# Optimization experiments

Measured on AMD Instinct MI355X. Metric: run time of the kernel, lower is better.

Reference implementation:

```python
import jax, jax.numpy as jnp
import numpy as np

# Math of ExampleModelSISO (in float; GMACv2 with unit scalars reduces to add,
# GMACv2([x],[y],[]) to elementwise multiply, CastToPrecision to identity):
#   states s_i (i=0..num_states-1) all init to zeros and all update identically:
#       s_i[t+1] = x[t] + s_i[t]
#   per-step output is x[t] * s_last[t], where s_last[t] = sum_{k<t} x[k]
#   i.e. out[t] = x[t] * exclusive_cumsum(x)[t]  (over the time axis).
# All num_states states are identical, so the scan collapses to one exclusive
# cumulative sum along time — fully vectorized, memory-bound.

def setup_inputs() -> dict:
    key = jax.random.key(0)
    B, T, D = 8, 4096, 1024
    x = jax.random.normal(key, (B, T, D), dtype=jnp.float32)
    return {"x": x}

def reference(x) -> jnp.ndarray:
    # exclusive cumulative sum over time axis (state before current input is added)
    prev_state = jnp.cumsum(x, axis=1) - x  # [B, T, D]
    return x * prev_state
```

## Files before the change

### kernel.cpp

```cpp
#include <hip/hip_runtime.h>


typedef float vf4 __attribute__((ext_vector_type(4)));

constexpr int B = 8;
constexpr int T = 4096;
constexpr int D = 1024;
constexpr int C = 128;
constexpr int L = T / C;
constexpr int THREADS = 256;
constexpr int BD = B * D;

__global__ __launch_bounds__(THREADS)
void partial_sums(const float* __restrict__ x, float* __restrict__ part) {
    const int bc = blockIdx.x;
    const int b = bc / C;
    const int c = bc % C;
    const int d4 = threadIdx.x * 4;

    const float* px = x + ((size_t)(b * T + c * L)) * D + d4;
    vf4 acc = (vf4)(0.f);
#pragma unroll 8
    for (int t = 0; t < L; ++t) {
        vf4 v = *(const vf4*)(px + (size_t)t * D);
        acc += v;
    }
    *(vf4*)(part + (size_t)c * BD + b * D + d4) = acc;
}

__global__ __launch_bounds__(THREADS)
void scan_partials(float* __restrict__ part) {
    const int j = blockIdx.x * blockDim.x + threadIdx.x;
    float run = 0.f;
    constexpr int TILE = 16;
#pragma unroll
    for (int c0 = 0; c0 < C; c0 += TILE) {
        float v[TILE];
#pragma unroll
        for (int k = 0; k < TILE; ++k)
            v[k] = part[(size_t)(c0 + k) * BD + j];
#pragma unroll
        for (int k = 0; k < TILE; ++k) {
            part[(size_t)(c0 + k) * BD + j] = run;
            run += v[k];
        }
    }
}

__global__ __launch_bounds__(THREADS)
void scan_mul(const float* __restrict__ x, const float* __restrict__ part,
              float* __restrict__ out) {
    const int bc = blockIdx.x;
    const int b = bc / C;
    const int c = bc % C;
    const int d4 = threadIdx.x * 4;

    const size_t base = ((size_t)(b * T + c * L)) * D + d4;
    vf4 s = *(const vf4*)(part + (size_t)c * BD + b * D + d4);
#pragma unroll 4
    for (int t = 0; t < L; ++t) {
        vf4 v = *(const vf4*)(x + base + (size_t)t * D);
        vf4 o = v * s;
        s += v;
        __builtin_nontemporal_store(o, (vf4*)(out + base + (size_t)t * D));
    }
}

extern "C" void kernel_launch(void* const* d_in, const int* in_sizes, int n_in,
                              void* d_out, int out_size, void* d_ws, size_t ws_size,
                              hipStream_t stream) {
    const float* x = (const float*)d_in[0];
    float* out = (float*)d_out;
    float* part = (float*)d_ws;

    partial_sums<<<B * C, THREADS, 0, stream>>>(x, part);
    scan_partials<<<BD / THREADS, THREADS, 0, stream>>>(part);
    scan_mul<<<B * C, THREADS, 0, stream>>>(x, part, out);
}
```

Baseline: 254.4 us.

## Replace three-pass scan with single-pass decoupled look-back scan

Merges the partial-sum, partial-scan and multiply kernels into one kernel. Chunks are assigned through an atomic ticket counter, and each chunk publishes a flagged aggregate or inclusive prefix in 64-bit slots that later chunks poll with a look-back. The second read of x for a chunk happens right after its first read, so it is likely served from cache, which aims to remove most of the extra full pass over x and two kernel launches. In exchange it adds an init kernel to clear the flags, spin-waiting on predecessors with a bounded retry count, and larger workspace traffic from the 64-bit slots.

```diff
diff --git a/kernel.cpp b/kernel.cpp
--- a/kernel.cpp
+++ b/kernel.cpp
@@ -9,71 +9,134 @@
 constexpr int C = 128;
 constexpr int L = T / C;
 constexpr int THREADS = 256;
-constexpr int BD = B * D;
+constexpr int NCHUNK = B * C;
+
+constexpr unsigned FLAG_INVALID = 0u;
+constexpr unsigned FLAG_AGG     = 1u;
+constexpr unsigned FLAG_PREFIX  = 2u;
+
 
 __global__ __launch_bounds__(THREADS)
-void partial_sums(const float* __restrict__ x, float* __restrict__ part) {
-    const int bc = blockIdx.x;
-    const int b = bc / C;
-    const int c = bc % C;
-    const int d4 = threadIdx.x * 4;
-
-    const float* px = x + ((size_t)(b * T + c * L)) * D + d4;
-    vf4 acc = (vf4)(0.f);
-#pragma unroll 8
-    for (int t = 0; t < L; ++t) {
-        vf4 v = *(const vf4*)(px + (size_t)t * D);
-        acc += v;
-    }
-    *(vf4*)(part + (size_t)c * BD + b * D + d4) = acc;
+void init_state(unsigned long long* __restrict__ slots,
+                unsigned* __restrict__ counter) {
+    const size_t i = (size_t)blockIdx.x * THREADS + threadIdx.x;
+#pragma unroll
+    for (int k = 0; k < 4; ++k)
+        slots[i * 4 + k] = 0ULL;
+    if (i == 0) *counter = 0u;
 }
 
 __global__ __launch_bounds__(THREADS)
-void scan_partials(float* __restrict__ part) {
-    const int j = blockIdx.x * blockDim.x + threadIdx.x;
-    float run = 0.f;
-    constexpr int TILE = 16;
+void scan_lookback(const float* __restrict__ x, float* __restrict__ out,
+                   unsigned long long* __restrict__ slots,
+                   unsigned* __restrict__ counter) {
+    __shared__ unsigned s_ticket;
+    if (threadIdx.x == 0) s_ticket = atomicAdd(counter, 1u);
+    __syncthreads();
+    const unsigned v = s_ticket;
+    const int b = (int)(v & (B - 1));
+    const int c = (int)(v >> 3);
+    const int d4 = threadIdx.x * 4;
+
+    const size_t xbase = ((size_t)(b * T + c * L)) * D + d4;
+
+    vf4 agg = (vf4)(0.f);
+#pragma unroll 8
+    for (int t = 0; t < L; ++t)
+        agg += *(const vf4*)(x + xbase + (size_t)t * D);
+
+    unsigned long long* myslot = slots + ((size_t)c * B + b) * D + d4;
+    {
+        const unsigned long long f =
+            (unsigned long long)(c == 0 ? FLAG_PREFIX : FLAG_AGG) << 32;
 #pragma unroll
-    for (int c0 = 0; c0 < C; c0 += TILE) {
-        float v[TILE];
-#pragma unroll
-        for (int k = 0; k < TILE; ++k)
-            v[k] = part[(size_t)(c0 + k) * BD + j];
-#pragma unroll
-        for (int k = 0; k < TILE; ++k) {
-            part[(size_t)(c0 + k) * BD + j] = run;
-            run += v[k];
+        for (int j = 0; j < 4; ++j) {
+            unsigned long long pk =
+                f | (unsigned long long)__float_as_uint(agg[j]);
+            __hip_atomic_store(&myslot[j], pk, __ATOMIC_RELAXED,
+                               __HIP_MEMORY_SCOPE_AGENT);
         }
     }
-}
 
-__global__ __launch_bounds__(THREADS)
-void scan_mul(const float* __restrict__ x, const float* __restrict__ part,
-              float* __restrict__ out) {
-    const int bc = blockIdx.x;
-    const int b = bc / C;
-    const int c = bc % C;
-    const int d4 = threadIdx.x * 4;
+    float pref[4] = {0.f, 0.f, 0.f, 0.f};
+    if (c > 0) {
+        int P = c - 1;
+        unsigned pend = 0xFu;
+        unsigned rounds = 0u;
+        while (pend) {
+            if (++rounds > (1u << 22)) break;
+            unsigned long long sv[4][4];
+#pragma unroll
+            for (int k = 0; k < 4; ++k) {
+                int p = P - k;
+                p = p < 0 ? 0 : p;
+                const unsigned long long* ps =
+                    slots + ((size_t)p * B + b) * D + d4;
+#pragma unroll
+                for (int j = 0; j < 4; ++j)
+                    sv[k][j] = __hip_atomic_load(&ps[j], __ATOMIC_RELAXED,
+                                                 __HIP_MEMORY_SCOPE_AGENT);
+            }
+            int consumed = 0;
+            bool halt = false;
+#pragma unroll
+            for (int k = 0; k < 4; ++k) {
+                const bool active = !halt && (P - k >= 0) && (pend != 0u);
+                if (active) {
+                    unsigned rdy = 1u;
+#pragma unroll
+                    for (int j = 0; j < 4; ++j)
+                        if ((pend >> j) & 1u)
+                            if ((unsigned)(sv[k][j] >> 32) == FLAG_INVALID)
+                                rdy = 0u;
+                    if (!rdy) {
+                        halt = true;
+                    } else {
+#pragma unroll
+                        for (int j = 0; j < 4; ++j)
+                            if ((pend >> j) & 1u) {
+                                pref[j] += __uint_as_float(
+                                    (unsigned)(sv[k][j] & 0xffffffffULL));
+                                if ((unsigned)(sv[k][j] >> 32) == FLAG_PREFIX)
+                                    pend &= ~(1u << j);
+                            }
+                        ++consumed;
+                    }
+                }
+            }
+            P -= consumed;
+            if (consumed == 0 && pend) __builtin_amdgcn_s_sleep(1);
+        }
+        const unsigned long long f = (unsigned long long)FLAG_PREFIX << 32;
+#pragma unroll
+        for (int j = 0; j < 4; ++j) {
+            unsigned long long pk =
+                f | (unsigned long long)__float_as_uint(pref[j] + agg[j]);
+            __hip_atomic_store(&myslot[j], pk, __ATOMIC_RELAXED,
+                               __HIP_MEMORY_SCOPE_AGENT);
+        }
+    }
 
-    const size_t base = ((size_t)(b * T + c * L)) * D + d4;
-    vf4 s = *(const vf4*)(part + (size_t)c * BD + b * D + d4);
+    vf4 s;
+    s[0] = pref[0]; s[1] = pref[1]; s[2] = pref[2]; s[3] = pref[3];
 #pragma unroll 4
     for (int t = 0; t < L; ++t) {
-        vf4 v = *(const vf4*)(x + base + (size_t)t * D);
-        vf4 o = v * s;
-        s += v;
-        __builtin_nontemporal_store(o, (vf4*)(out + base + (size_t)t * D));
+        vf4 vv = *(const vf4*)(x + xbase + (size_t)t * D);
+        vf4 o = vv * s;
+        s += vv;
+        __builtin_nontemporal_store(o, (vf4*)(out + xbase + (size_t)t * D));
     }
 }
 
 extern "C" void kernel_launch(void* const* d_in, const int* in_sizes, int n_in,
-                              void* d_out, int out_size, void* d_ws, size_t ws_size,
-                              hipStream_t stream) {
+                              void* d_out, int out_size, void* d_ws,
+                              size_t ws_size, hipStream_t stream) {
     const float* x = (const float*)d_in[0];
     float* out = (float*)d_out;
-    float* part = (float*)d_ws;
+    unsigned long long* slots = (unsigned long long*)d_ws;
+    unsigned* counter =
+        (unsigned*)((char*)d_ws + (size_t)NCHUNK * D * sizeof(unsigned long long));
 
-    partial_sums<<<B * C, THREADS, 0, stream>>>(x, part);
-    scan_partials<<<BD / THREADS, THREADS, 0, stream>>>(part);
-    scan_mul<<<B * C, THREADS, 0, stream>>>(x, part, out);
+    init_state<<<1024, THREADS, 0, stream>>>(slots, counter);
+    scan_lookback<<<NCHUNK, THREADS, 0, stream>>>(x, out, slots, counter);
 }
```

Measured after the change: 612.3 us. 141% more time.

## Fuse three scan kernels into one cooperative kernel with grid syncs

Applied to the files above, without the earlier changes.

Merges the partial-sum, partial-scan and scan-multiply kernels into a single cooperative launch separated by two grid-wide barriers. This removes two kernel launch gaps. Each block's chunk of x may also still be in L2/MALL when it is reread in the final pass. In exchange it adds grid.sync overhead, and only 32 of the 1024 blocks do the middle scan while the rest wait. The cooperative launch also requires all blocks to be co-resident.

```diff
diff --git a/kernel.cpp b/kernel.cpp
--- a/kernel.cpp
+++ b/kernel.cpp
@@ -1,7 +1,10 @@
 #include <hip/hip_runtime.h>
+#include <hip/hip_cooperative_groups.h>
 
 
 typedef float vf4 __attribute__((ext_vector_type(4)));
+
+namespace cg = cooperative_groups;
 
 constexpr int B = 8;
 constexpr int T = 4096;
@@ -10,70 +13,66 @@
 constexpr int L = T / C;
 constexpr int THREADS = 256;
 constexpr int BD = B * D;
+constexpr int NBLK = B * C;
 
 __global__ __launch_bounds__(THREADS)
-void partial_sums(const float* __restrict__ x, float* __restrict__ part) {
+void fused_scan(const float* __restrict__ x, float* __restrict__ part,
+                float* __restrict__ out) {
+    cg::grid_group grid = cg::this_grid();
+
     const int bc = blockIdx.x;
     const int b = bc / C;
     const int c = bc % C;
     const int d4 = threadIdx.x * 4;
 
-    const float* px = x + ((size_t)(b * T + c * L)) * D + d4;
-    vf4 acc = (vf4)(0.f);
+    const size_t xbase = ((size_t)(b * T + c * L)) * D + d4;
+
+    vf4 agg = (vf4)(0.f);
 #pragma unroll 8
-    for (int t = 0; t < L; ++t) {
-        vf4 v = *(const vf4*)(px + (size_t)t * D);
-        acc += v;
-    }
-    *(vf4*)(part + (size_t)c * BD + b * D + d4) = acc;
-}
+    for (int t = 0; t < L; ++t)
+        agg += *(const vf4*)(x + xbase + (size_t)t * D);
+    *(vf4*)(part + (size_t)c * BD + b * D + d4) = agg;
 
-__global__ __launch_bounds__(THREADS)
-void scan_partials(float* __restrict__ part) {
-    const int j = blockIdx.x * blockDim.x + threadIdx.x;
-    float run = 0.f;
-    constexpr int TILE = 16;
+    grid.sync();
+
+    if (bc < BD / THREADS) {
+        const int j = bc * THREADS + threadIdx.x;
+        float run = 0.f;
+        constexpr int TILE = 16;
 #pragma unroll
-    for (int c0 = 0; c0 < C; c0 += TILE) {
-        float v[TILE];
+        for (int c0 = 0; c0 < C; c0 += TILE) {
+            float v[TILE];
 #pragma unroll
-        for (int k = 0; k < TILE; ++k)
-            v[k] = part[(size_t)(c0 + k) * BD + j];
+            for (int k = 0; k < TILE; ++k)
+                v[k] = part[(size_t)(c0 + k) * BD + j];
 #pragma unroll
-        for (int k = 0; k < TILE; ++k) {
-            part[(size_t)(c0 + k) * BD + j] = run;
-            run += v[k];
+            for (int k = 0; k < TILE; ++k) {
+                part[(size_t)(c0 + k) * BD + j] = run;
+                run += v[k];
+            }
         }
     }
-}
 
-__global__ __launch_bounds__(THREADS)
-void scan_mul(const float* __restrict__ x, const float* __restrict__ part,
-              float* __restrict__ out) {
-    const int bc = blockIdx.x;
-    const int b = bc / C;
-    const int c = bc % C;
-    const int d4 = threadIdx.x * 4;
+    grid.sync();
 
-    const size_t base = ((size_t)(b * T + c * L)) * D + d4;
     vf4 s = *(const vf4*)(part + (size_t)c * BD + b * D + d4);
 #pragma unroll 4
     for (int t = 0; t < L; ++t) {
-        vf4 v = *(const vf4*)(x + base + (size_t)t * D);
+        vf4 v = *(const vf4*)(x + xbase + (size_t)t * D);
         vf4 o = v * s;
         s += v;
-        __builtin_nontemporal_store(o, (vf4*)(out + base + (size_t)t * D));
+        __builtin_nontemporal_store(o, (vf4*)(out + xbase + (size_t)t * D));
     }
 }
 
 extern "C" void kernel_launch(void* const* d_in, const int* in_sizes, int n_in,
-                              void* d_out, int out_size, void* d_ws, size_t ws_size,
-                              hipStream_t stream) {
+                              void* d_out, int out_size, void* d_ws,
+                              size_t ws_size, hipStream_t stream) {
     const float* x = (const float*)d_in[0];
     float* out = (float*)d_out;
     float* part = (float*)d_ws;
 
-    partial_sums<<<B * C, THREADS, 0, stream>>>(x, part);
-    scan_partials<<<BD / THREADS, THREADS, 0, stream>>>(part);
-    scan_mul<<<B * C, THREADS, 0, stream>>>(x, part, out);
+    void* args[] = {(void*)&x, (void*)&part, (void*)&out};
+    hipLaunchCooperativeKernel((const void*)fused_scan, dim3(NBLK),
+                               dim3(THREADS), args, 0, stream);
 }
```

Result: slower. 485.7 us (+90.9%).

## Fold partial-sum scan into scan_mul and halve chunk count

Applied to the files above, without the earlier changes.

Drops the separate scan_partials kernel. Each scan_mul block now computes its own exclusive prefix by summing the preceding chunk partials directly, using four independent accumulators. Chunk count goes from 128 to 64, so chunks are longer, and the unroll factors go up. This removes one kernel launch and a serial pass over the partials, at the cost of redundant partial reads per block (up to 63 vf4 loads) and half as many blocks, which means less parallelism.

```diff
diff --git a/kernel.cpp b/kernel.cpp
--- a/kernel.cpp
+++ b/kernel.cpp
@@ -6,10 +6,10 @@
 constexpr int B = 8;
 constexpr int T = 4096;
 constexpr int D = 1024;
-constexpr int C = 128;
+constexpr int C = 64;
 constexpr int L = T / C;
 constexpr int THREADS = 256;
-constexpr int BD = B * D;
+
 
 __global__ __launch_bounds__(THREADS)
 void partial_sums(const float* __restrict__ x, float* __restrict__ part) {
@@ -20,31 +20,10 @@
 
     const float* px = x + ((size_t)(b * T + c * L)) * D + d4;
     vf4 acc = (vf4)(0.f);
-#pragma unroll 8
-    for (int t = 0; t < L; ++t) {
-        vf4 v = *(const vf4*)(px + (size_t)t * D);
-        acc += v;
-    }
-    *(vf4*)(part + (size_t)c * BD + b * D + d4) = acc;
-}
-
-__global__ __launch_bounds__(THREADS)
-void scan_partials(float* __restrict__ part) {
-    const int j = blockIdx.x * blockDim.x + threadIdx.x;
-    float run = 0.f;
-    constexpr int TILE = 16;
-#pragma unroll
-    for (int c0 = 0; c0 < C; c0 += TILE) {
-        float v[TILE];
-#pragma unroll
-        for (int k = 0; k < TILE; ++k)
-            v[k] = part[(size_t)(c0 + k) * BD + j];
-#pragma unroll
-        for (int k = 0; k < TILE; ++k) {
-            part[(size_t)(c0 + k) * BD + j] = run;
-            run += v[k];
-        }
-    }
+#pragma unroll 16
+    for (int t = 0; t < L; ++t)
+        acc += *(const vf4*)(px + (size_t)t * D);
+    *(vf4*)(part + ((size_t)c * B + b) * D + d4) = acc;
 }
 
 __global__ __launch_bounds__(THREADS)
@@ -55,9 +34,23 @@
     const int c = bc % C;
     const int d4 = threadIdx.x * 4;
 
+    vf4 s0 = (vf4)(0.f), s1 = (vf4)(0.f), s2 = (vf4)(0.f), s3 = (vf4)(0.f);
+    {
+        const float* pp = part + (size_t)b * D + d4;
+        int p = 0;
+        for (; p + 4 <= c; p += 4) {
+            s0 += *(const vf4*)(pp + (size_t)(p + 0) * B * D);
+            s1 += *(const vf4*)(pp + (size_t)(p + 1) * B * D);
+            s2 += *(const vf4*)(pp + (size_t)(p + 2) * B * D);
+            s3 += *(const vf4*)(pp + (size_t)(p + 3) * B * D);
+        }
+        for (; p < c; ++p)
+            s0 += *(const vf4*)(pp + (size_t)p * B * D);
+    }
+    vf4 s = (s0 + s1) + (s2 + s3);
+
     const size_t base = ((size_t)(b * T + c * L)) * D + d4;
-    vf4 s = *(const vf4*)(part + (size_t)c * BD + b * D + d4);
-#pragma unroll 4
+#pragma unroll 8
     for (int t = 0; t < L; ++t) {
         vf4 v = *(const vf4*)(x + base + (size_t)t * D);
         vf4 o = v * s;
@@ -74,6 +67,5 @@
     float* part = (float*)d_ws;
 
     partial_sums<<<B * C, THREADS, 0, stream>>>(x, part);
-    scan_partials<<<BD / THREADS, THREADS, 0, stream>>>(part);
     scan_mul<<<B * C, THREADS, 0, stream>>>(x, part, out);
 }
```

Result: faster. 248.9 us, median of 2 (-2.2%).
